# Performance work log

Hardware: AMD Instinct MI355X
Metric: run time of the kernel (lower is better)

## Reference

```python
import jax, jax.numpy as jnp
import numpy as np

TARGET_RADIUS = 0.99
EPS = 1e-8


def _effective_W_h(W_h):
    """Spectral-norm constraint: 3 power iterations (no grad through u,v),
    then rescale W_h so its spectral radius is TARGET_RADIUS."""
    dim = W_h.shape[0]
    u = jax.random.normal(jax.random.key(1), (dim,), dtype=W_h.dtype)
    u = u / jnp.linalg.norm(u)
    Ws = jax.lax.stop_gradient(W_h)
    v = None
    for _ in range(3):
        v = Ws.T @ u
        v = v / (jnp.linalg.norm(v) + EPS)
        u = Ws @ v
        u = u / (jnp.linalg.norm(u) + EPS)
    sigma = jnp.abs(u @ W_h @ v)  # grad flows only through W_h here
    return W_h * (TARGET_RADIUS / (sigma + EPS))


def setup_inputs() -> dict:
    key = jax.random.key(0)
    ks = jax.random.split(key, 6)
    T, B, D = 2048, 16, 1024
    xavier = float(np.sqrt(6.0 / (D + D)))
    return {
        "x": jax.random.normal(ks[0], (T, B, D), dtype=jnp.float32),
        "h0": jnp.zeros((B, D), dtype=jnp.float32),
        "W_x": jax.random.uniform(ks[1], (D, D), jnp.float32, -xavier, xavier),
        "W_h": jax.random.uniform(ks[2], (D, D), jnp.float32, -xavier, xavier),
        "W_delta": jax.random.uniform(ks[3], (D, D), jnp.float32, -0.1 * xavier, 0.1 * xavier),
        "b": jnp.zeros((D,), dtype=jnp.float32),
        "b_delta": jnp.full((D,), -2.0, dtype=jnp.float32),
        "b_gate": jnp.zeros((D,), dtype=jnp.float32),
    }


def reference(x, h0, W_x, W_h, W_delta, b, b_delta, b_gate):
    # x: [T, B, D]; h0: [B, D]
    W_h_eff = _effective_W_h(W_h)
    # Batch the input-side GEMMs over all timesteps at once.
    delta_raw = jnp.einsum("tbd,ed->tbe", x, W_delta) + b_delta  # [T,B,D]
    cand_x = jnp.einsum("tbd,ed->tbe", x, W_x) + b               # [T,B,D]

    def step(h_prev, inputs):
        x_t, dr_t, cx_t = inputs
        delta = jax.nn.sigmoid(dr_t)
        candidate = jnp.tanh(cx_t + h_prev @ W_h_eff.T)
        h_new = (1.0 - delta) * h_prev + delta * candidate
        out_t = h_new * jax.nn.silu(h_new + x_t + b_gate)
        return h_new, (out_t, h_new)

    _, (output, hs) = jax.lax.scan(step, h0, (x, delta_raw, cand_x))
    h = jnp.concatenate([h0[None], hs], axis=0)  # [T+1, B, D]
    return output, h
```

## Files before the change

### kernel.cpp

```cpp
#include <hip/hip_runtime.h>
#include <hip/hip_fp16.h>
#include <stdint.h>

#define TT 2048
#define BB 16
#define DD 1024
static const size_t H0OFF = 33554432;

typedef _Float16 f16;
typedef _Float16 f16x2 __attribute__((ext_vector_type(2)));
typedef _Float16 f16x8 __attribute__((ext_vector_type(8)));
typedef float f32x4 __attribute__((ext_vector_type(4)));

__device__ __forceinline__ float erfinv_xla(float x) {
  float w = -log1pf(-x * x);
  float p;
  if (w < 5.0f) {
    w -= 2.5f;
    p = 2.81022636e-08f;
    p = fmaf(p, w, 3.43273939e-07f);
    p = fmaf(p, w, -3.5233877e-06f);
    p = fmaf(p, w, -4.39150654e-06f);
    p = fmaf(p, w, 0.00021858087f);
    p = fmaf(p, w, -0.00125372503f);
    p = fmaf(p, w, -0.00417768164f);
    p = fmaf(p, w, 0.246640727f);
    p = fmaf(p, w, 1.50140941f);
  } else {
    w = sqrtf(w) - 3.0f;
    p = -0.000200214257f;
    p = fmaf(p, w, 0.000100950558f);
    p = fmaf(p, w, 0.00134934322f);
    p = fmaf(p, w, -0.00367342844f);
    p = fmaf(p, w, 0.00573950773f);
    p = fmaf(p, w, -0.0076224613f);
    p = fmaf(p, w, 0.00943887047f);
    p = fmaf(p, w, 1.00167406f);
    p = fmaf(p, w, 2.83297682f);
  }
  return p * x;
}

__device__ __forceinline__ float bits_to_normal(unsigned bits) {
  unsigned fb = (bits >> 9) | 0x3f800000u;
  float f = __uint_as_float(fb) - 1.0f;
  const float lo = -0.99999994f;
  float u = f * 2.0f + lo;
  u = fmaxf(lo, u);
  return __uint_as_float(0x3fb504f3u) * erfinv_xla(u);
}

#define TF_ROUND(r) { x0 += x1; x1 = (x1 << r) | (x1 >> (32 - r)); x1 ^= x0; }

__global__ void k_u0(float* t0, float* u) {
  __shared__ float red[512];
  int i = threadIdx.x;
  unsigned ks0 = 0u, ks1 = 1u, ks2 = 0x1BD11BDAu ^ 0u ^ 1u;
  unsigned x0 = (unsigned)i + ks0;
  unsigned x1 = (unsigned)(i + 512) + ks1;
  TF_ROUND(13) TF_ROUND(15) TF_ROUND(26) TF_ROUND(6)
  x0 += ks1; x1 += ks2 + 1u;
  TF_ROUND(17) TF_ROUND(29) TF_ROUND(16) TF_ROUND(24)
  x0 += ks2; x1 += ks0 + 2u;
  TF_ROUND(13) TF_ROUND(15) TF_ROUND(26) TF_ROUND(6)
  x0 += ks0; x1 += ks1 + 3u;
  TF_ROUND(17) TF_ROUND(29) TF_ROUND(16) TF_ROUND(24)
  x0 += ks1; x1 += ks2 + 4u;
  TF_ROUND(13) TF_ROUND(15) TF_ROUND(26) TF_ROUND(6)
  x0 += ks2; x1 += ks0 + 5u;
  float z0 = bits_to_normal(x0);
  float z1 = bits_to_normal(x1);
  t0[i] = z0; t0[i + 512] = z1;
  red[i] = z0 * z0 + z1 * z1;
  __syncthreads();
  for (int s = 256; s > 0; s >>= 1) { if (i < s) red[i] += red[i + s]; __syncthreads(); }
  float inv = 1.0f / sqrtf(red[0]);
  u[i] = t0[i] * inv; u[i + 512] = t0[i + 512] * inv;
}

__global__ void k_mvT(const float* __restrict__ W, const float* __restrict__ u,
                      float* __restrict__ out) {
  int j = blockIdx.x * 256 + threadIdx.x;
  float acc = 0.f;
  for (int i = 0; i < DD; ++i) acc = fmaf(W[(size_t)i * DD + j], u[i], acc);
  out[j] = acc;
}

__global__ void k_mv(const float* __restrict__ W, const float* __restrict__ v,
                     float* __restrict__ out) {
  int gtid = blockIdx.x * 256 + threadIdx.x;
  int wave = gtid >> 6, lane = threadIdx.x & 63;
  for (int rr = 0; rr < 16; ++rr) {
    int row = wave * 16 + rr;
    float acc = 0.f;
    for (int c = 0; c < 16; ++c) {
      int col = c * 64 + lane;
      acc = fmaf(W[(size_t)row * DD + col], v[col], acc);
    }
    for (int off = 32; off > 0; off >>= 1) acc += __shfl_down(acc, off, 64);
    if (lane == 0) out[row] = acc;
  }
}

__global__ void k_norm(const float* __restrict__ src, float* __restrict__ dst, float eps) {
  __shared__ float red[1024];
  int i = threadIdx.x;
  float xv = src[i];
  red[i] = xv * xv;
  __syncthreads();
  for (int s = 512; s > 0; s >>= 1) { if (i < s) red[i] += red[i + s]; __syncthreads(); }
  float inv = 1.0f / (sqrtf(red[0]) + eps);
  dst[i] = src[i] * inv;
}

__global__ void k_sigma(const float* __restrict__ u, const float* __restrict__ wv,
                        float* __restrict__ scale) {
  __shared__ float red[1024];
  int i = threadIdx.x;
  red[i] = u[i] * wv[i];
  __syncthreads();
  for (int s = 512; s > 0; s >>= 1) { if (i < s) red[i] += red[i + s]; __syncthreads(); }
  if (i == 0) scale[0] = 0.99f / (fabsf(red[0]) + 1e-8f);
}

__global__ void k_castWh(const float* __restrict__ Wh, const float* __restrict__ scale,
                         f16* __restrict__ WhH) {
  int i = blockIdx.x * 256 + threadIdx.x;
  float s = scale[0];
  WhH[i] = (f16)(Wh[i] * s);
}

__global__ __launch_bounds__(256) void k_gemm(const float* __restrict__ X,
                                              const float* __restrict__ Wt,
                                              const float* __restrict__ bias,
                                              float* __restrict__ Cout) {
  __shared__ __align__(16) f16 Ah[128 * 64];
  __shared__ __align__(16) f16 Bh[128 * 64];
  int m0 = blockIdx.x * 128, n0 = blockIdx.y * 128;
  int tid = threadIdx.x, lane = tid & 63, w = tid >> 6;
  int wm = w & 1, wn = w >> 1;
  int srow = tid >> 3, scol = (tid & 7) * 8;
  f32x4 acc[4][4];
#pragma unroll
  for (int i = 0; i < 4; ++i)
#pragma unroll
    for (int j = 0; j < 4; ++j) acc[i][j] = (f32x4){0.f, 0.f, 0.f, 0.f};

  for (int kt = 0; kt < 16; ++kt) {
    int k0 = kt * 64;
#pragma unroll
    for (int c = 0; c < 4; ++c) {
      int row = c * 32 + srow;
      const float4* sa = (const float4*)(X + (size_t)(m0 + row) * DD + k0 + scol);
      float4 a0 = sa[0], a1 = sa[1];
      f16x8 hv;
      hv[0] = (f16)a0.x; hv[1] = (f16)a0.y; hv[2] = (f16)a0.z; hv[3] = (f16)a0.w;
      hv[4] = (f16)a1.x; hv[5] = (f16)a1.y; hv[6] = (f16)a1.z; hv[7] = (f16)a1.w;
      *(f16x8*)&Ah[row * 64 + scol] = hv;
      const float4* sb = (const float4*)(Wt + (size_t)(n0 + row) * DD + k0 + scol);
      float4 b0 = sb[0], b1 = sb[1];
      f16x8 hw;
      hw[0] = (f16)b0.x; hw[1] = (f16)b0.y; hw[2] = (f16)b0.z; hw[3] = (f16)b0.w;
      hw[4] = (f16)b1.x; hw[5] = (f16)b1.y; hw[6] = (f16)b1.z; hw[7] = (f16)b1.w;
      *(f16x8*)&Bh[row * 64 + scol] = hw;
    }
    __syncthreads();
#pragma unroll
    for (int ks = 0; ks < 2; ++ks) {
      f16x8 af[4], bf[4];
#pragma unroll
      for (int i = 0; i < 4; ++i)
        af[i] = *(const f16x8*)&Ah[(wm * 64 + i * 16 + (lane & 15)) * 64 + ks * 32 + (lane >> 4) * 8];
#pragma unroll
      for (int j = 0; j < 4; ++j)
        bf[j] = *(const f16x8*)&Bh[(wn * 64 + j * 16 + (lane & 15)) * 64 + ks * 32 + (lane >> 4) * 8];
#pragma unroll
      for (int i = 0; i < 4; ++i)
#pragma unroll
        for (int j = 0; j < 4; ++j)
          acc[i][j] = __builtin_amdgcn_mfma_f32_16x16x32_f16(af[i], bf[j], acc[i][j], 0, 0, 0);
    }
    __syncthreads();
  }
#pragma unroll
  for (int j = 0; j < 4; ++j) {
    int col = n0 + wn * 64 + j * 16 + (lane & 15);
    float bs = bias[col];
#pragma unroll
    for (int i = 0; i < 4; ++i) {
      int rbase = m0 + wm * 64 + i * 16 + (lane >> 4) * 4;
#pragma unroll
      for (int r = 0; r < 4; ++r)
        Cout[(size_t)(rbase + r) * DD + col] = acc[i][j][r] + bs;
    }
  }
}

__device__ __forceinline__ float fdot2u(uint32_t a, uint32_t b, float c) {
#if __has_builtin(__builtin_amdgcn_fdot2)
  return __builtin_amdgcn_fdot2(__builtin_bit_cast(f16x2, a),
                                __builtin_bit_cast(f16x2, b), c, false);
#else
  f16x2 av = __builtin_bit_cast(f16x2, a), bv = __builtin_bit_cast(f16x2, b);
  return c + (float)av[0] * (float)bv[0] + (float)av[1] * (float)bv[1];
#endif
}

__device__ __forceinline__ float sigmoid_fast(float v) {
  return 1.0f / (1.0f + __expf(-v));
}
__device__ __forceinline__ float tanh_fast(float v) {
  float t = __expf(-2.0f * fabsf(v));
  float r = (1.0f - t) / (1.0f + t);
  return copysignf(r, v);
}

__global__ __launch_bounds__(256, 1) void k_rec(const float* __restrict__ x,
                                                const float* __restrict__ h0,
                                                const float* __restrict__ b_gate,
                                                const f16* __restrict__ WhH,
                                                uint32_t* __restrict__ hx,
                                                float* __restrict__ d_out) {
  int bid = blockIdx.x;
  int batch = bid & 15;
  int eslice = bid >> 4;
  int tid = threadIdx.x, lane = tid & 63, wv = tid >> 6;

  __shared__ __align__(16) uint16_t hsh[1024];
  __shared__ float partial[2][4][64];

  uint4 wq[32];
  {
    const uint4* wp = (const uint4*)(WhH + (size_t)(64 * eslice + lane) * DD + 256 * wv);
#pragma unroll
    for (int k = 0; k < 32; ++k) wq[k] = wp[k];
  }

#pragma unroll
  for (int k = 0; k < 4; ++k) {
    int g = 256 * wv + 64 * k + lane;
    hsh[g] = __builtin_bit_cast(uint16_t, (f16)h0[(size_t)batch * DD + g]);
  }

  float h_own = 0.f, bgv = 0.f, cx_c = 0.f, dr_c = 0.f, xv_c = 0.f;
  int e_g = 0;
  if (lane < 16) {
    int rr = 16 * wv + lane;
    e_g = 64 * eslice + rr;
    size_t b0 = (size_t)batch * DD + e_g;
    h_own = h0[b0];
    bgv = b_gate[e_g];
    d_out[H0OFF + b0] = h_own;
    cx_c = d_out[b0];
    dr_c = d_out[H0OFF + 16384 + b0];
    xv_c = x[b0];
  }
  asm volatile("s_waitcnt lgkmcnt(0)" ::: "memory");

#pragma unroll 1
  for (int t = 0; t < TT; ++t) {
    float cx_n = 0.f, dr_n = 0.f, xv_n = 0.f;
    if (lane < 16 && t + 1 < TT) {
      size_t bn = (size_t)(t + 1) * 16384 + (size_t)batch * DD + e_g;
      cx_n = d_out[bn];
      dr_n = d_out[H0OFF + 16384 + bn];
      xv_n = x[bn];
    }

    const uint4* hq = (const uint4*)hsh;
    float a0 = 0.f, a1 = 0.f, a2 = 0.f, a3 = 0.f;
#pragma unroll
    for (int k = 0; k < 32; k += 4) {
      {
        uint4 q = hq[32 * wv + k + 0]; uint4 wqq = wq[k + 0];
        a0 = fdot2u(wqq.x, q.x, a0); a0 = fdot2u(wqq.y, q.y, a0);
        a0 = fdot2u(wqq.z, q.z, a0); a0 = fdot2u(wqq.w, q.w, a0);
      }
      {
        uint4 q = hq[32 * wv + k + 1]; uint4 wqq = wq[k + 1];
        a1 = fdot2u(wqq.x, q.x, a1); a1 = fdot2u(wqq.y, q.y, a1);
        a1 = fdot2u(wqq.z, q.z, a1); a1 = fdot2u(wqq.w, q.w, a1);
      }
      {
        uint4 q = hq[32 * wv + k + 2]; uint4 wqq = wq[k + 2];
        a2 = fdot2u(wqq.x, q.x, a2); a2 = fdot2u(wqq.y, q.y, a2);
        a2 = fdot2u(wqq.z, q.z, a2); a2 = fdot2u(wqq.w, q.w, a2);
      }
      {
        uint4 q = hq[32 * wv + k + 3]; uint4 wqq = wq[k + 3];
        a3 = fdot2u(wqq.x, q.x, a3); a3 = fdot2u(wqq.y, q.y, a3);
        a3 = fdot2u(wqq.z, q.z, a3); a3 = fdot2u(wqq.w, q.w, a3);
      }
    }
    partial[t & 1][wv][lane] = (a0 + a1) + (a2 + a3);
    __syncthreads();

    uint32_t want = (uint32_t)(t + 1);
    uint32_t* sl = hx + (size_t)(want & 15u) * (BB * DD) + (size_t)batch * DD;

    if (lane < 16) {
      int rr = 16 * wv + lane;
      const float* pp = &partial[t & 1][0][rr];
      float hdot = (pp[0] + pp[64]) + (pp[128] + pp[192]);
      float dlt = sigmoid_fast(dr_c);
      float cand = tanh_fast(cx_c + hdot);
      float hn = (1.f - dlt) * h_own + dlt * cand;
      uint16_t hb = __builtin_bit_cast(uint16_t, (f16)hn);
      __hip_atomic_store(&sl[e_g], (want << 16) | (uint32_t)hb,
                         __ATOMIC_RELAXED, __HIP_MEMORY_SCOPE_AGENT);
      size_t base = (size_t)t * 16384 + (size_t)batch * DD + e_g;
      float z = hn + xv_c + bgv;
      d_out[base] = hn * z * sigmoid_fast(z);
      d_out[H0OFF + 16384 + base] = hn;
      h_own = hn; cx_c = cx_n; dr_c = dr_n; xv_c = xv_n;
    }

    if (t + 1 < TT) {
      int sidx = 256 * wv + 64 * (lane >> 2) + 16 * (lane & 3);
      while (true) {
        uint32_t swd = (lane < 16)
            ? __hip_atomic_load(&sl[sidx], __ATOMIC_RELAXED, __HIP_MEMORY_SCOPE_AGENT)
            : (want << 16);
        if (__all((swd >> 16) == want)) break;
        __builtin_amdgcn_s_sleep(1);
      }
      uint32_t v0, v1, v2, v3;
      while (true) {
        v0 = __hip_atomic_load(&sl[256 * wv + lane],       __ATOMIC_RELAXED, __HIP_MEMORY_SCOPE_AGENT);
        v1 = __hip_atomic_load(&sl[256 * wv + 64 + lane],  __ATOMIC_RELAXED, __HIP_MEMORY_SCOPE_AGENT);
        v2 = __hip_atomic_load(&sl[256 * wv + 128 + lane], __ATOMIC_RELAXED, __HIP_MEMORY_SCOPE_AGENT);
        v3 = __hip_atomic_load(&sl[256 * wv + 192 + lane], __ATOMIC_RELAXED, __HIP_MEMORY_SCOPE_AGENT);
        bool ok = ((v0 >> 16) == want) & ((v1 >> 16) == want) &
                  ((v2 >> 16) == want) & ((v3 >> 16) == want);
        if (__all(ok)) break;
        __builtin_amdgcn_s_sleep(1);
      }
      hsh[256 * wv + lane]       = (uint16_t)v0;
      hsh[256 * wv + 64 + lane]  = (uint16_t)v1;
      hsh[256 * wv + 128 + lane] = (uint16_t)v2;
      hsh[256 * wv + 192 + lane] = (uint16_t)v3;
      asm volatile("s_waitcnt lgkmcnt(0)" ::: "memory");
    }
  }
}

extern "C" void kernel_launch(void* const* d_in, const int* in_sizes, int n_in,
                              void* d_out_v, int out_size, void* d_ws, size_t ws_size,
                              hipStream_t stream) {
  const float* x  = (const float*)d_in[0];
  const float* h0 = (const float*)d_in[1];
  const float* Wx = (const float*)d_in[2];
  const float* Wh = (const float*)d_in[3];
  const float* Wd = (const float*)d_in[4];
  const float* b  = (const float*)d_in[5];
  const float* bd = (const float*)d_in[6];
  const float* bg = (const float*)d_in[7];
  float* out = (float*)d_out_v;

  char* ws = (char*)d_ws;
  float* u    = (float*)(ws + 0);
  float* v    = (float*)(ws + 4096);
  float* t0   = (float*)(ws + 8192);
  float* sc   = (float*)(ws + 12288);
  uint32_t* hx = (uint32_t*)(ws + 65536);
  f16* WhH  = (f16*)(ws + 2097152);

  hipMemsetAsync(hx, 0, (size_t)16 * BB * DD * 4, stream);

  k_u0<<<1, 512, 0, stream>>>(t0, u);
  for (int it = 0; it < 3; ++it) {
    k_mvT<<<4, 256, 0, stream>>>(Wh, u, t0);
    k_norm<<<1, 1024, 0, stream>>>(t0, v, 1e-8f);
    k_mv<<<16, 256, 0, stream>>>(Wh, v, t0);
    k_norm<<<1, 1024, 0, stream>>>(t0, u, 1e-8f);
  }
  k_sigma<<<1, 1024, 0, stream>>>(u, t0, sc);
  k_castWh<<<4096, 256, 0, stream>>>(Wh, sc, WhH);

  dim3 gg(256, 8, 1);
  k_gemm<<<gg, 256, 0, stream>>>(x, Wx, b, out);
  k_gemm<<<gg, 256, 0, stream>>>(x, Wd, bd, out + H0OFF + 16384);

  k_rec<<<256, 256, 0, stream>>>(x, h0, bg, WhH, hx, out);
}
```

Baseline: 4.890 ms.

## Stage W_h in swizzled LDS and overlap per-chunk polling with dot products

Each block now copies its 64-row slice of the fp16 recurrent weight into a bank-swizzled shared-memory buffer instead of holding it in registers. Per step, polling for the next hidden state is split into four 64-element chunks, and each chunk's partial dot product starts as soon as that chunk arrives. Polling uses sc0 loads with no sleep. The block-to-(batch, slice) mapping is changed so that all 16 slices of one batch share the same bid&7, which is meant to keep their exchange inside one XCD's L2. The changes trade register pressure for LDS traffic and reorder the step computation, which adds risk around correctness of the cross-block handoff.

```diff
diff --git a/kernel.cpp b/kernel.cpp
--- a/kernel.cpp
+++ b/kernel.cpp
@@ -215,6 +215,42 @@
   return copysignf(r, v);
 }
 
+__device__ __forceinline__ uint32_t load_sc0(const uint32_t* p) {
+  uint32_t v;
+  asm volatile("global_load_dword %0, %1, off sc0\n\ts_waitcnt vmcnt(0)"
+               : "=v"(v) : "v"(p) : "memory");
+  return v;
+}
+
+__device__ __forceinline__ uint32_t poll_word(const uint32_t* wp, uint32_t want) {
+  uint32_t v;
+  int it = 0;
+  while (true) {
+    if ((it & 7) != 7) {
+      v = load_sc0(wp);
+    } else {
+      v = __hip_atomic_load(wp, __ATOMIC_RELAXED, __HIP_MEMORY_SCOPE_AGENT);
+    }
+    if (__all((v >> 16) == want)) break;
+    ++it;
+  }
+  return v;
+}
+
+__device__ __forceinline__ float dot256(const uint4 w[8], const uint4* hq4, int b16) {
+  float ac[4] = {0.f, 0.f, 0.f, 0.f};
+#pragma unroll
+  for (int j = 0; j < 8; ++j) {
+    uint4 hh = hq4[b16 + j];
+    uint4 ww = w[j];
+    float a = ac[j & 3];
+    a = fdot2u(ww.x, hh.x, a); a = fdot2u(ww.y, hh.y, a);
+    a = fdot2u(ww.z, hh.z, a); a = fdot2u(ww.w, hh.w, a);
+    ac[j & 3] = a;
+  }
+  return (ac[0] + ac[1]) + (ac[2] + ac[3]);
+}
+
 __global__ __launch_bounds__(256, 1) void k_rec(const float* __restrict__ x,
                                                 const float* __restrict__ h0,
                                                 const float* __restrict__ b_gate,
@@ -222,31 +258,38 @@
                                                 uint32_t* __restrict__ hx,
                                                 float* __restrict__ d_out) {
   int bid = blockIdx.x;
-  int batch = bid & 15;
-  int eslice = bid >> 4;
+  int batch = (bid & 7) + ((bid >> 7) << 3);
+  int eslice = (bid >> 3) & 15;
   int tid = threadIdx.x, lane = tid & 63, wv = tid >> 6;
 
+  __shared__ __align__(16) f16 Wsh[64 * 1024];
   __shared__ __align__(16) uint16_t hsh[1024];
   __shared__ float partial[2][4][64];
 
-  uint4 wq[32];
   {
-    const uint4* wp = (const uint4*)(WhH + (size_t)(64 * eslice + lane) * DD + 256 * wv);
-#pragma unroll
-    for (int k = 0; k < 32; ++k) wq[k] = wp[k];
-  }
-
-#pragma unroll
-  for (int k = 0; k < 4; ++k) {
-    int g = 256 * wv + 64 * k + lane;
-    hsh[g] = __builtin_bit_cast(uint16_t, (f16)h0[(size_t)batch * DD + g]);
+    int r = tid >> 2, q = tid & 3;
+    const uint4* src = (const uint4*)(WhH + (size_t)(64 * eslice + r) * DD + q * 256);
+    uint4* dst = (uint4*)Wsh;
+#pragma unroll
+    for (int j = 0; j < 32; ++j) {
+      int cc = q * 32 + j;
+      dst[r * 128 + (cc ^ (r & 7))] = src[j];
+    }
+  }
+  {
+    const float4* hb = (const float4*)(h0 + (size_t)batch * DD) + tid;
+    float4 a = *hb;
+    ushort4 pk;
+    pk.x = __builtin_bit_cast(uint16_t, (f16)a.x);
+    pk.y = __builtin_bit_cast(uint16_t, (f16)a.y);
+    pk.z = __builtin_bit_cast(uint16_t, (f16)a.z);
+    pk.w = __builtin_bit_cast(uint16_t, (f16)a.w);
+    *(ushort4*)&hsh[4 * tid] = pk;
   }
 
   float h_own = 0.f, bgv = 0.f, cx_c = 0.f, dr_c = 0.f, xv_c = 0.f;
-  int e_g = 0;
+  int e_g = 64 * eslice + 16 * wv + (lane & 15);
   if (lane < 16) {
-    int rr = 16 * wv + lane;
-    e_g = 64 * eslice + rr;
     size_t b0 = (size_t)batch * DD + e_g;
     h_own = h0[b0];
     bgv = b_gate[e_g];
@@ -255,44 +298,26 @@
     dr_c = d_out[H0OFF + 16384 + b0];
     xv_c = x[b0];
   }
-  asm volatile("s_waitcnt lgkmcnt(0)" ::: "memory");
+  __syncthreads();
+
+  const uint4* Wsh4 = (const uint4*)Wsh;
+  const uint4* hq4 = (const uint4*)hsh;
+
+  {
+    float p = 0.f;
+#pragma unroll
+    for (int s = 0; s < 4; ++s) {
+      uint4 w[8];
+#pragma unroll
+      for (int j = 0; j < 8; ++j)
+        w[j] = Wsh4[lane * 128 + ((32 * wv + 8 * s + j) ^ (lane & 7))];
+      p += dot256(w, hq4, 32 * wv + 8 * s);
+    }
+    partial[0][wv][lane] = p;
+  }
 
 #pragma unroll 1
   for (int t = 0; t < TT; ++t) {
-    float cx_n = 0.f, dr_n = 0.f, xv_n = 0.f;
-    if (lane < 16 && t + 1 < TT) {
-      size_t bn = (size_t)(t + 1) * 16384 + (size_t)batch * DD + e_g;
-      cx_n = d_out[bn];
-      dr_n = d_out[H0OFF + 16384 + bn];
-      xv_n = x[bn];
-    }
-
-    const uint4* hq = (const uint4*)hsh;
-    float a0 = 0.f, a1 = 0.f, a2 = 0.f, a3 = 0.f;
-#pragma unroll
-    for (int k = 0; k < 32; k += 4) {
-      {
-        uint4 q = hq[32 * wv + k + 0]; uint4 wqq = wq[k + 0];
-        a0 = fdot2u(wqq.x, q.x, a0); a0 = fdot2u(wqq.y, q.y, a0);
-        a0 = fdot2u(wqq.z, q.z, a0); a0 = fdot2u(wqq.w, q.w, a0);
-      }
-      {
-        uint4 q = hq[32 * wv + k + 1]; uint4 wqq = wq[k + 1];
-        a1 = fdot2u(wqq.x, q.x, a1); a1 = fdot2u(wqq.y, q.y, a1);
-        a1 = fdot2u(wqq.z, q.z, a1); a1 = fdot2u(wqq.w, q.w, a1);
-      }
-      {
-        uint4 q = hq[32 * wv + k + 2]; uint4 wqq = wq[k + 2];
-        a2 = fdot2u(wqq.x, q.x, a2); a2 = fdot2u(wqq.y, q.y, a2);
-        a2 = fdot2u(wqq.z, q.z, a2); a2 = fdot2u(wqq.w, q.w, a2);
-      }
-      {
-        uint4 q = hq[32 * wv + k + 3]; uint4 wqq = wq[k + 3];
-        a3 = fdot2u(wqq.x, q.x, a3); a3 = fdot2u(wqq.y, q.y, a3);
-        a3 = fdot2u(wqq.z, q.z, a3); a3 = fdot2u(wqq.w, q.w, a3);
-      }
-    }
-    partial[t & 1][wv][lane] = (a0 + a1) + (a2 + a3);
     __syncthreads();
 
     uint32_t want = (uint32_t)(t + 1);
@@ -304,42 +329,44 @@
       float hdot = (pp[0] + pp[64]) + (pp[128] + pp[192]);
       float dlt = sigmoid_fast(dr_c);
       float cand = tanh_fast(cx_c + hdot);
-      float hn = (1.f - dlt) * h_own + dlt * cand;
+      float hn = fmaf(dlt, cand - h_own, h_own);
       uint16_t hb = __builtin_bit_cast(uint16_t, (f16)hn);
-      __hip_atomic_store(&sl[e_g], (want << 16) | (uint32_t)hb,
-                         __ATOMIC_RELAXED, __HIP_MEMORY_SCOPE_AGENT);
+      uint32_t tagged = (want << 16) | (uint32_t)hb;
+      __hip_atomic_store(&sl[e_g], tagged, __ATOMIC_RELAXED, __HIP_MEMORY_SCOPE_AGENT);
+      *(volatile uint32_t*)&sl[e_g] = tagged;
       size_t base = (size_t)t * 16384 + (size_t)batch * DD + e_g;
       float z = hn + xv_c + bgv;
       d_out[base] = hn * z * sigmoid_fast(z);
       d_out[H0OFF + 16384 + base] = hn;
-      h_own = hn; cx_c = cx_n; dr_c = dr_n; xv_c = xv_n;
+      h_own = hn;
+      if (t + 1 < TT) {
+        size_t bn = (size_t)(t + 1) * 16384 + (size_t)batch * DD + e_g;
+        cx_c = d_out[bn];
+        dr_c = d_out[H0OFF + 16384 + bn];
+        xv_c = x[bn];
+      }
     }
 
     if (t + 1 < TT) {
-      int sidx = 256 * wv + 64 * (lane >> 2) + 16 * (lane & 3);
-      while (true) {
-        uint32_t swd = (lane < 16)
-            ? __hip_atomic_load(&sl[sidx], __ATOMIC_RELAXED, __HIP_MEMORY_SCOPE_AGENT)
-            : (want << 16);
-        if (__all((swd >> 16) == want)) break;
-        __builtin_amdgcn_s_sleep(1);
+      uint4 wA[8], wB[8];
+#pragma unroll
+      for (int j = 0; j < 8; ++j)
+        wA[j] = Wsh4[lane * 128 + ((32 * wv + j) ^ (lane & 7))];
+      float psum = 0.f;
+#pragma unroll
+      for (int s = 0; s < 4; ++s) {
+        uint32_t v = poll_word(sl + 256 * wv + 64 * s + lane, want);
+        if (s < 3) {
+#pragma unroll
+          for (int j = 0; j < 8; ++j)
+            wB[j] = Wsh4[lane * 128 + ((32 * wv + 8 * (s + 1) + j) ^ (lane & 7))];
+        }
+        hsh[256 * wv + 64 * s + lane] = (uint16_t)v;
+        psum += dot256(wA, hq4, 32 * wv + 8 * s);
+#pragma unroll
+        for (int j = 0; j < 8; ++j) wA[j] = wB[j];
       }
-      uint32_t v0, v1, v2, v3;
-      while (true) {
-        v0 = __hip_atomic_load(&sl[256 * wv + lane],       __ATOMIC_RELAXED, __HIP_MEMORY_SCOPE_AGENT);
-        v1 = __hip_atomic_load(&sl[256 * wv + 64 + lane],  __ATOMIC_RELAXED, __HIP_MEMORY_SCOPE_AGENT);
-        v2 = __hip_atomic_load(&sl[256 * wv + 128 + lane], __ATOMIC_RELAXED, __HIP_MEMORY_SCOPE_AGENT);
-        v3 = __hip_atomic_load(&sl[256 * wv + 192 + lane], __ATOMIC_RELAXED, __HIP_MEMORY_SCOPE_AGENT);
-        bool ok = ((v0 >> 16) == want) & ((v1 >> 16) == want) &
-                  ((v2 >> 16) == want) & ((v3 >> 16) == want);
-        if (__all(ok)) break;
-        __builtin_amdgcn_s_sleep(1);
-      }
-      hsh[256 * wv + lane]       = (uint16_t)v0;
-      hsh[256 * wv + 64 + lane]  = (uint16_t)v1;
-      hsh[256 * wv + 128 + lane] = (uint16_t)v2;
-      hsh[256 * wv + 192 + lane] = (uint16_t)v3;
-      asm volatile("s_waitcnt lgkmcnt(0)" ::: "memory");
+      partial[(t + 1) & 1][wv][lane] = psum;
     }
   }
 }
```

Measured after the change: 6.313 ms. 1.29x slower.
